# Kernel optimization log

Hardware: AMD Instinct MI355X
Metric: run time of the kernel (lower is better)

Reference implementation:

```python
import jax, jax.numpy as jnp
import numpy as np

# ---- neuron / simulation params (network.yaml analogue) ----
THETA = 10.0      # spike threshold
TAU_SR = 4.0      # SRM (psp) kernel time constant
TAU_REF = 4.0     # refractory kernel time constant
SCALE_REF = 2.0
TS = 1.0          # simulation step
T_SAMPLE = 1000
N_BATCH, N_IN, N_OUT = 16, 2048, 512
SPIKE_RATE = 0.1


def _alpha_kernel(tau, mult, eps_cut):
    # SLAYER _calculateAlphaKernel: truncated alpha function samples
    vals = []
    for t in np.arange(0.0, T_SAMPLE, TS):
        v = mult * t / tau * np.exp(1.0 - t / tau)
        if abs(v) < eps_cut and t > tau:
            break
        vals.append(v)
    return np.asarray(vals, dtype=np.float32)

SRM_KERNEL = _alpha_kernel(TAU_SR, 1.0, 0.01)
REF_KERNEL = _alpha_kernel(TAU_REF, -SCALE_REF * THETA, 0.0001)  # fullRefKernel=True
# pending-refractory shift vector: refKernel[0]==0 is consumed at spike time
REF_SHIFT = jnp.asarray(np.concatenate([REF_KERNEL[1:], [0.0]]).astype(np.float32))


def psp(spike_in):
    # causal temporal filter: psp[n,c,t] = Ts * sum_j srm[j] * s[n,c,t-j]
    N, C, T = spike_in.shape
    Ls = SRM_KERNEL.shape[0]
    x = spike_in.reshape(N * C, 1, T)
    k = jnp.asarray(SRM_KERNEL)[::-1].reshape(1, 1, Ls)  # flip -> convolution
    y = jax.lax.conv_general_dilated(
        x, k, window_strides=(1,), padding=[(Ls - 1, 0)],
        dimension_numbers=('NCH', 'OIH', 'NCH'))
    return y.reshape(N, C, T) * TS


def spike_scan(wpsp):
    # sequential spike generation with refractory feedback (SLAYER getSpikes)
    N, C, T = wpsp.shape
    L = REF_SHIFT.shape[0]

    def step(buf, x):
        u = x + buf[..., 0]                       # membrane incl. past refractory
        ind = (u >= THETA).astype(x.dtype)
        buf = jnp.concatenate([buf[..., 1:], jnp.zeros_like(buf[..., :1])], -1) \
              + ind[..., None] * REF_SHIFT        # schedule refractory for future t
        return buf, (ind / TS, u)

    buf0 = jnp.zeros((N, C, L), wpsp.dtype)
    _, (s, u) = jax.lax.scan(step, buf0, jnp.moveaxis(wpsp, -1, 0))
    return jnp.moveaxis(s, 0, -1), jnp.moveaxis(u, 0, -1)


def setup_inputs() -> dict:
    key = jax.random.key(0)
    k1, k2 = jax.random.split(key)
    spikeInput = (jax.random.uniform(k1, (N_BATCH, N_IN, T_SAMPLE)) < SPIKE_RATE
                  ).astype(jnp.float32)
    weight = jax.random.normal(k2, (N_OUT, N_IN), dtype=jnp.float32) * 0.3
    return {'spikeInput': spikeInput, 'weight': weight}


def reference(spikeInput, weight):
    p = psp(spikeInput)                           # [N, Nin, T]
    wpsp = jnp.einsum('oi,nit->not', weight, p)   # 1x1x1 conv == matmul, no bias
    spikes, _ = spike_scan(wpsp)                  # [N, Nout, T]
    return spikes
```

## Files before the change

### kernel.cpp

```cpp
#include <hip/hip_runtime.h>
#include <hip/hip_bf16.h>
#include <math.h>

#define NB 16
#define NIN 2048
#define NOUT 512
#define TT 1000
#define L_SRM 31

typedef int v4i  __attribute__((ext_vector_type(4)));
typedef int v16i __attribute__((ext_vector_type(16)));

__device__ __forceinline__ unsigned long long spread8(unsigned int b) {
    unsigned long long x = (unsigned long long)(b & 0xFFu) * 0x0101010101010101ULL;
    x &= 0x8040201008040201ULL;
    x |= x >> 4; x |= x >> 2; x |= x >> 1;
    return x & 0x0101010101010101ULL;
}

__global__ __launch_bounds__(256) void k_quant(const float* __restrict__ W,
                                               signed char* __restrict__ Bq) {
    int idx = blockIdx.x * 256 + threadIdx.x;
    int o = idx >> 11, i = idx & (NIN - 1);
    double w = (double)W[o * NIN + i];
    int wq = (int)rint(w * 536870912.0);
    int b0 = (int)(signed char)(wq & 255); int r = (wq - b0) >> 8;
    int b1 = (int)(signed char)(r  & 255); r = (r - b1) >> 8;
    int b2 = (int)(signed char)(r  & 255); r = (r - b2) >> 8;
    int b3 = r;
    size_t e = (size_t)o * NIN + i;
    Bq[e]                = (signed char)b0;
    Bq[e + 1048576]      = (signed char)b1;
    Bq[e + 2097152]      = (signed char)b2;
    Bq[e + 3145728]      = (signed char)b3;
}

__global__ __launch_bounds__(256) void k_extract(const float* __restrict__ s,
                                                 unsigned long long* __restrict__ bits) {
    __shared__ float tile[64][65];
    int tc = blockIdx.x, ic = blockIdx.y, n = blockIdx.z;
    int t0 = tc * 64, i0 = ic * 64;
    int tid = threadIdx.x;
    int r = tid >> 2, cq = tid & 3;
    const float* rp = s + ((size_t)(n * NIN + i0 + r)) * TT + t0;
    #pragma unroll
    for (int q = 0; q < 4; ++q) {
        int col = cq * 16 + q * 4;
        float4 v = make_float4(0.f, 0.f, 0.f, 0.f);
        if (t0 + col + 3 < TT) v = *(const float4*)(rp + col);
        tile[r][col] = v.x; tile[r][col + 1] = v.y;
        tile[r][col + 2] = v.z; tile[r][col + 3] = v.w;
    }
    __syncthreads();
    int lane = tid & 63, w = tid >> 6;
    #pragma unroll
    for (int k = 0; k < 16; ++k) {
        int tl = w * 16 + k;
        if (t0 + tl >= TT) break;
        unsigned long long m = __ballot(tile[lane][tl] != 0.0f);
        if (lane == 0) bits[((size_t)n * TT + t0 + tl) * 32 + ic] = m;
    }
}

__global__ __launch_bounds__(512) void k_spmm(const unsigned long long* __restrict__ bits,
                                              const signed char* __restrict__ Bq,
                                              double* __restrict__ z) {
    __shared__ char Alds[128 * 128];
    __shared__ char Blds[4][64 * 128];
    int tid = threadIdx.x;
    int bid = blockIdx.x;
    int o0  = (bid & 7) * 64;
    int nt0 = (bid >> 3) * 128;

    const int arow_w = tid >> 2, q = tid & 3;
    const int p_st = tid >> 7, orow = (tid >> 1) & 63, h = tid & 1;
    const unsigned int* agp = (const unsigned int*)bits + (size_t)(nt0 + arow_w) * 64 + q;
    const signed char*  bgp = Bq + (size_t)p_st * (NOUT * NIN)
                                 + (size_t)(o0 + orow) * NIN + h * 64;
    char* awp = Alds + arow_w * 128;
    const int xra_w = arow_w & 7;
    char* bwp = Blds[p_st] + orow * 128;
    const int xro_w = orow & 7;

    const int l = tid & 63, wv = tid >> 6;
    const int wm = wv >> 1, wn = wv & 1;
    const int arow = wm * 32 + (l & 31), xra = arow & 7;
    const int brow = wn * 32 + (l & 31), xrb = brow & 7;
    const int kg = l >> 5;

    v16i acc0 = {}, acc1 = {}, acc2 = {}, acc3 = {};

    unsigned int aw = agp[0];
    int4 bs0 = ((const int4*)bgp)[0], bs1 = ((const int4*)bgp)[1],
         bs2 = ((const int4*)bgp)[2], bs3 = ((const int4*)bgp)[3];

    for (int ks = 0; ks < 16; ++ks) {
        __syncthreads();
        {
            unsigned long long s0 = spread8(aw), s1 = spread8(aw >> 8),
                               s2 = spread8(aw >> 16), s3 = spread8(aw >> 24);
            ulonglong2 v0; v0.x = s0; v0.y = s1;
            ulonglong2 v1; v1.x = s2; v1.y = s3;
            *(ulonglong2*)(awp + (((2 * q)     ^ xra_w) << 4)) = v0;
            *(ulonglong2*)(awp + (((2 * q + 1) ^ xra_w) << 4)) = v1;
            *(int4*)(bwp + (((h * 4 + 0) ^ xro_w) << 4)) = bs0;
            *(int4*)(bwp + (((h * 4 + 1) ^ xro_w) << 4)) = bs1;
            *(int4*)(bwp + (((h * 4 + 2) ^ xro_w) << 4)) = bs2;
            *(int4*)(bwp + (((h * 4 + 3) ^ xro_w) << 4)) = bs3;
        }
        __syncthreads();
        if (ks < 15) {
            aw = agp[(ks + 1) * 4];
            const int4* g = (const int4*)(bgp + (size_t)(ks + 1) * 128);
            bs0 = g[0]; bs1 = g[1]; bs2 = g[2]; bs3 = g[3];
        }
        #pragma unroll
        for (int ksub = 0; ksub < 4; ++ksub) {
            int ca = ksub * 2 + kg;
            v4i av  = *(const v4i*)(Alds    + arow * 128 + (((ca) ^ xra) << 4));
            v4i bv0 = *(const v4i*)(Blds[0] + brow * 128 + (((ca) ^ xrb) << 4));
            v4i bv1 = *(const v4i*)(Blds[1] + brow * 128 + (((ca) ^ xrb) << 4));
            v4i bv2 = *(const v4i*)(Blds[2] + brow * 128 + (((ca) ^ xrb) << 4));
            v4i bv3 = *(const v4i*)(Blds[3] + brow * 128 + (((ca) ^ xrb) << 4));
            acc0 = __builtin_amdgcn_mfma_i32_32x32x32_i8(av, bv0, acc0, 0, 0, 0);
            acc1 = __builtin_amdgcn_mfma_i32_32x32x32_i8(av, bv1, acc1, 0, 0, 0);
            acc2 = __builtin_amdgcn_mfma_i32_32x32x32_i8(av, bv2, acc2, 0, 0, 0);
            acc3 = __builtin_amdgcn_mfma_i32_32x32x32_i8(av, bv3, acc3, 0, 0, 0);
        }
    }

    #pragma unroll
    for (int r = 0; r < 16; ++r) {
        int row = (r & 3) + 8 * (r >> 2) + 4 * kg;
        long long tot = ((long long)acc3[r] << 24) + ((long long)acc2[r] << 16)
                      + ((long long)acc1[r] << 8)  +  (long long)acc0[r];
        double zv = (double)tot * (1.0 / 536870912.0);
        __builtin_nontemporal_store(zv,
            &z[(size_t)(nt0 + wm * 32 + row) * NOUT + (o0 + wn * 32 + (l & 31))]);
    }
}

__global__ __launch_bounds__(128) void k_conv(const double* __restrict__ z,
                                              double* __restrict__ wpsp) {
    __shared__ float srm_s[32];
    __shared__ __align__(16) double zs[62 * 128];
    int tid = threadIdx.x;
    if (tid < L_SRM) {
        double t = (double)tid;
        srm_s[tid] = (float)((t / 4.0) * exp(1.0 - t / 4.0));
    }
    int tb = blockIdx.x * 32;
    int oc = blockIdx.y * 128;
    int n  = blockIdx.z;
    const double* zp = z + ((size_t)n * TT) * NOUT + oc;
    int wv = tid >> 6, lane = tid & 63;
    for (int r = wv; r < 62; r += 2) {
        int t = tb - 30 + r;
        if (t >= 0 && t < TT) {
            const double* src = zp + (size_t)t * NOUT + lane * 2;
            __builtin_amdgcn_global_load_lds(
                (const __attribute__((address_space(1))) void*)src,
                (__attribute__((address_space(3))) void*)(&zs[r * 128]),
                16, 0, 0);
        } else {
            double2 zero; zero.x = 0.0; zero.y = 0.0;
            *(double2*)(&zs[r * 128 + lane * 2]) = zero;
        }
    }
    asm volatile("s_waitcnt vmcnt(0)" ::: "memory");
    __syncthreads();
    for (int tl = 0; tl < 32; ++tl) {
        int t = tb + tl;
        if (t >= TT) break;
        double a0 = 0., a1 = 0., a2 = 0., a3 = 0.;
        #pragma unroll
        for (int jj = 0; jj < 28; jj += 4) {
            a0 += (double)srm_s[jj]     * zs[(tl + 30 - jj) * 128 + tid];
            a1 += (double)srm_s[jj + 1] * zs[(tl + 29 - jj) * 128 + tid];
            a2 += (double)srm_s[jj + 2] * zs[(tl + 28 - jj) * 128 + tid];
            a3 += (double)srm_s[jj + 3] * zs[(tl + 27 - jj) * 128 + tid];
        }
        a0 += (double)srm_s[28] * zs[(tl + 2) * 128 + tid];
        a1 += (double)srm_s[29] * zs[(tl + 1) * 128 + tid];
        a2 += (double)srm_s[30] * zs[(tl + 0) * 128 + tid];
        wpsp[((size_t)n * TT + t) * NOUT + oc + tid] = (a0 + a1) + (a2 + a3);
    }
}

__global__ __launch_bounds__(64) void k_scan(const double* __restrict__ wpsp,
                                             float* __restrict__ out) {
    __shared__ float  refTab[64];
    __shared__ double Tb[8][256];
    int lane = threadIdx.x;
    {
        double d = (double)lane;
        refTab[lane] = (lane == 0) ? 0.0f
                     : (float)(-20.0 * (d / 4.0) * exp(1.0 - d / 4.0));
    }
    __syncthreads();
    for (int e = lane; e < 2048; e += 64) {
        int k = e >> 8, m = e & 255;
        double s = 0.0;
        #pragma unroll
        for (int j = 0; j < 8; ++j) {
            int idx = 8 * k + j + 1;
            if (((m >> j) & 1) && idx <= 63) s += (double)refTab[idx];
        }
        Tb[k][m] = s;
    }
    __syncthreads();

    int n  = blockIdx.x >> 3;
    int o0 = (blockIdx.x & 7) << 6;
    const double* xsrc = wpsp + ((size_t)n * TT) * NOUT + o0 + lane;
    float* op = out + ((size_t)(n * NOUT) + o0 + lane) * TT;
    const double* Tb0 = &Tb[0][0];

    double xp = xsrc[0];
    double x1 = xsrc[NOUT];
    double xq[8];
    #pragma unroll
    for (int j = 0; j < 8; ++j) xq[(j + 2) & 7] = xsrc[(size_t)(j + 2) * NOUT];

    unsigned long long h = 0ULL;
    bool sp1 = false;
    double p0 = 0., p1 = 0., p2 = 0., p3 = 0., p4 = 0., p5 = 0., p6 = 0.;
    double e0 = 0.0, e1 = 0.0;
    double c1_0 = Tb0[0], c1_1 = Tb0[1], c1_2 = Tb0[2], c1_3 = Tb0[3];

    for (int tb = 0; tb < TT; tb += 8) {
        unsigned omask = 0;
        #pragma unroll
        for (int tl = 0; tl < 8; ++tl) {
            int t = tb + tl;
            h = (h << 1) | (unsigned long long)sp1;
            unsigned long long hs = h << 2;
            double q1 = Tb[1][(unsigned)((hs >>  8) & 255)];
            double q2 = Tb[2][(unsigned)((hs >> 16) & 255)];
            double q3 = Tb[3][(unsigned)((hs >> 24) & 255)];
            double q4 = Tb[4][(unsigned)((hs >> 32) & 255)];
            double q5 = Tb[5][(unsigned)((hs >> 40) & 255)];
            double q6 = Tb[6][(unsigned)((hs >> 48) & 255)];
            double q7 = Tb[7][(unsigned)((hs >> 56) & 255)];
            unsigned m = (unsigned)(hs & 255);
            double2 nc01 = *(const double2*)(Tb0 + m);
            double2 nc23 = *(const double2*)(Tb0 + m + 2);
            double nx = xq[(tl + 2) & 7];
            int tload = t + 10; if (tload > TT - 1) tload = TT - 1;
            xq[(tl + 2) & 7] = xsrc[(size_t)tload * NOUT];
            double e0n = sp1 ? c1_2 : c1_0;
            double e1n = sp1 ? c1_3 : c1_1;
            double np1 = ((p0 + p1) + (p2 + p3)) + ((p4 + p5) + p6);
            double u = xp + (sp1 ? e1 : e0);
            bool spt = (u >= 10.0);
            omask |= ((unsigned)spt) << tl;
            double nxp = x1 + np1;
            sp1 = spt; e0 = e0n; e1 = e1n;
            xp = nxp; x1 = nx;
            p0 = q1; p1 = q2; p2 = q3; p3 = q4; p4 = q5; p5 = q6; p6 = q7;
            c1_0 = nc01.x; c1_1 = nc01.y; c1_2 = nc23.x; c1_3 = nc23.y;
        }
        float4 v0, v1;
        v0.x = (omask & 1u)   ? 1.0f : 0.0f;  v0.y = (omask & 2u)   ? 1.0f : 0.0f;
        v0.z = (omask & 4u)   ? 1.0f : 0.0f;  v0.w = (omask & 8u)   ? 1.0f : 0.0f;
        v1.x = (omask & 16u)  ? 1.0f : 0.0f;  v1.y = (omask & 32u)  ? 1.0f : 0.0f;
        v1.z = (omask & 64u)  ? 1.0f : 0.0f;  v1.w = (omask & 128u) ? 1.0f : 0.0f;
        *(float4*)(op + tb)     = v0;
        *(float4*)(op + tb + 4) = v1;
    }
}

extern "C" void kernel_launch(void* const* d_in, const int* in_sizes, int n_in,
                              void* d_out, int out_size, void* d_ws, size_t ws_size,
                              hipStream_t stream) {
    const float* spikeInput = (const float*)d_in[0];
    const float* weight     = (const float*)d_in[1];
    float* out = (float*)d_out;

    char* ws = (char*)d_ws;
    unsigned long long* bits = (unsigned long long*)ws;
    signed char*        Bq   = (signed char*)(ws + 4194304);
    double*             z    = (double*)(ws + 8388608);
    double*             wpsp = (double*)(ws + 73924608);

    k_quant<<<(NOUT * NIN) / 256, 256, 0, stream>>>(weight, Bq);
    k_extract<<<dim3(16, 32, 16), 256, 0, stream>>>(spikeInput, bits);
    k_spmm<<<1000, 512, 0, stream>>>(bits, Bq, z);
    k_conv<<<dim3(32, 4, 16), 128, 0, stream>>>(z, wpsp);
    k_scan<<<128, 64, 0, stream>>>(wpsp, out);
}
```

Baseline: 482.2 us.

## Split refractory sum into block-old table lookups and in-block register terms

Restructures the sequential spike scan so that refractory contributions from spikes older than the current 8-step block are computed up front for all 8 steps using table lookups on the block-aligned history. Only contributions from the last 7 in-block spikes are resolved serially with register constants and selects. This is meant to take the shared-memory lookups off the serial dependence chain, at the cost of more selects and adds per step in the serial loop. The changed summation order in double precision could in rare cases shift threshold decisions.

```diff
diff --git a/kernel.cpp b/kernel.cpp
--- a/kernel.cpp
+++ b/kernel.cpp
@@ -210,56 +210,53 @@
     }
     __syncthreads();
 
+    const double K1 = (double)refTab[1], K2 = (double)refTab[2],
+                 K3 = (double)refTab[3], K4 = (double)refTab[4],
+                 K5 = (double)refTab[5], K6 = (double)refTab[6],
+                 K7 = (double)refTab[7], K8 = (double)refTab[8];
+
     int n  = blockIdx.x >> 3;
     int o0 = (blockIdx.x & 7) << 6;
     const double* xsrc = wpsp + ((size_t)n * TT) * NOUT + o0 + lane;
     float* op = out + ((size_t)(n * NOUT) + o0 + lane) * TT;
-    const double* Tb0 = &Tb[0][0];
-
-    double xp = xsrc[0];
-    double x1 = xsrc[NOUT];
+
     double xq[8];
     #pragma unroll
-    for (int j = 0; j < 8; ++j) xq[(j + 2) & 7] = xsrc[(size_t)(j + 2) * NOUT];
-
-    unsigned long long h = 0ULL;
-    bool sp1 = false;
-    double p0 = 0., p1 = 0., p2 = 0., p3 = 0., p4 = 0., p5 = 0., p6 = 0.;
-    double e0 = 0.0, e1 = 0.0;
-    double c1_0 = Tb0[0], c1_1 = Tb0[1], c1_2 = Tb0[2], c1_3 = Tb0[3];
+    for (int j = 0; j < 8; ++j) xq[j] = xsrc[(size_t)j * NOUT];
+
+    unsigned long long h0 = 0ULL;
+    unsigned mrec = 0;
 
     for (int tb = 0; tb < TT; tb += 8) {
+        double xold[8];
+        #pragma unroll
+        for (int tl = 0; tl < 8; ++tl) {
+            unsigned long long hs = h0 << tl;
+            double T1 = Tb[1][(unsigned)((hs >>  8) & 255)];
+            double T2 = Tb[2][(unsigned)((hs >> 16) & 255)];
+            double T3 = Tb[3][(unsigned)((hs >> 24) & 255)];
+            double T4 = Tb[4][(unsigned)((hs >> 32) & 255)];
+            double T5 = Tb[5][(unsigned)((hs >> 40) & 255)];
+            double T6 = Tb[6][(unsigned)((hs >> 48) & 255)];
+            double T7 = Tb[7][(unsigned)((hs >> 56) & 255)];
+            double T0 = (hs & 128ULL) ? K8 : 0.0;
+            double xv = xq[tl];
+            int tload = tb + tl + 8; if (tload > TT - 1) tload = TT - 1;
+            xq[tl] = xsrc[(size_t)tload * NOUT];
+            xold[tl] = xv + (((T0 + T1) + (T2 + T3)) + ((T4 + T5) + (T6 + T7)));
+        }
         unsigned omask = 0;
         #pragma unroll
         for (int tl = 0; tl < 8; ++tl) {
-            int t = tb + tl;
-            h = (h << 1) | (unsigned long long)sp1;
-            unsigned long long hs = h << 2;
-            double q1 = Tb[1][(unsigned)((hs >>  8) & 255)];
-            double q2 = Tb[2][(unsigned)((hs >> 16) & 255)];
-            double q3 = Tb[3][(unsigned)((hs >> 24) & 255)];
-            double q4 = Tb[4][(unsigned)((hs >> 32) & 255)];
-            double q5 = Tb[5][(unsigned)((hs >> 40) & 255)];
-            double q6 = Tb[6][(unsigned)((hs >> 48) & 255)];
-            double q7 = Tb[7][(unsigned)((hs >> 56) & 255)];
-            unsigned m = (unsigned)(hs & 255);
-            double2 nc01 = *(const double2*)(Tb0 + m);
-            double2 nc23 = *(const double2*)(Tb0 + m + 2);
-            double nx = xq[(tl + 2) & 7];
-            int tload = t + 10; if (tload > TT - 1) tload = TT - 1;
-            xq[(tl + 2) & 7] = xsrc[(size_t)tload * NOUT];
-            double e0n = sp1 ? c1_2 : c1_0;
-            double e1n = sp1 ? c1_3 : c1_1;
-            double np1 = ((p0 + p1) + (p2 + p3)) + ((p4 + p5) + p6);
-            double u = xp + (sp1 ? e1 : e0);
+            double rest7 = (((mrec & 2u)  ? K2 : 0.0) + ((mrec & 4u)  ? K3 : 0.0))
+                         + (((mrec & 8u)  ? K4 : 0.0) + ((mrec & 16u) ? K5 : 0.0))
+                         + (((mrec & 32u) ? K6 : 0.0) + ((mrec & 64u) ? K7 : 0.0));
+            double u = (xold[tl] + rest7) + ((mrec & 1u) ? K1 : 0.0);
             bool spt = (u >= 10.0);
             omask |= ((unsigned)spt) << tl;
-            double nxp = x1 + np1;
-            sp1 = spt; e0 = e0n; e1 = e1n;
-            xp = nxp; x1 = nx;
-            p0 = q1; p1 = q2; p2 = q3; p3 = q4; p4 = q5; p5 = q6; p6 = q7;
-            c1_0 = nc01.x; c1_1 = nc01.y; c1_2 = nc23.x; c1_3 = nc23.y;
-        }
+            mrec = (mrec << 1) | (unsigned)spt;
+        }
+        h0 = (h0 << 8) | (unsigned long long)(mrec & 255u);
         float4 v0, v1;
         v0.x = (omask & 1u)   ? 1.0f : 0.0f;  v0.y = (omask & 2u)   ? 1.0f : 0.0f;
         v0.z = (omask & 4u)   ? 1.0f : 0.0f;  v0.w = (omask & 8u)   ? 1.0f : 0.0f;
```

Result: slower. 501.9 us (+4.1%).
